# Performance work log

Hardware: AMD Instinct MI355X
Metric: run time of the kernel (lower is better)

The kernel has to match this reference:

```python
import jax, jax.numpy as jnp
import numpy as np

FFT_LEN = 256
WIN_LEN = 768
FRM_LEN = 128
PPF_TAP = WIN_LEN // FFT_LEN  # 6
SCALE = -256.0
GROUP_DELAY = 648  # module uses group_delay = -648
B, C, S, T = 8, 2, FFT_LEN // 2 + 1, 4096


def _make_lpf(win_len):
    # firwin(win_len, 0.5, window='hann', scale=False) equivalent
    n = np.arange(win_len, dtype=np.float64)
    w = 0.5 - 0.5 * np.cos(2.0 * np.pi * n / (win_len - 1))
    h = w * np.sinc(0.5 * (n - (win_len - 1) / 2.0))
    return jnp.asarray(h, dtype=jnp.float32)


def setup_inputs() -> dict:
    key = jax.random.key(0)
    k1, k2 = jax.random.split(key)
    spectrum_real = jax.random.normal(k1, (B, C, S, T), dtype=jnp.float32)
    spectrum_imag = jax.random.normal(k2, (B, C, S, T), dtype=jnp.float32)
    lpf_coef = _make_lpf(WIN_LEN)
    return {"spectrum_real": spectrum_real, "spectrum_imag": spectrum_imag, "lpf_coef": lpf_coef}


def reference(spectrum_real, spectrum_imag, lpf_coef):
    # spectrum: (B, C, S, T) complex; per-frame irfft over subbands
    spec = jnp.swapaxes(spectrum_real + 1j * spectrum_imag, -1, -2)  # (B,C,T,S)
    fftout = jnp.fft.irfft(spec, n=FFT_LEN, axis=-1)                 # (B,C,T,FFT_LEN)
    rev = fftout[..., ::-1]                                          # comp_in[fft_len-j-1]
    v = jnp.tile(rev, (1, 1, 1, PPF_TAP)) * lpf_coef                 # (B,C,T,WIN_LEN)
    b, c, t, _ = v.shape
    num_samples = t * FRM_LEN
    # overlap-add: frame t contributes v[t] at offset t*FRM_LEN (shifting buffer recurrence)
    idx = jnp.arange(t)[:, None] * FRM_LEN + jnp.arange(WIN_LEN)[None, :]  # (T, WIN_LEN)
    y = jnp.zeros((b, c, num_samples + WIN_LEN), dtype=v.dtype)
    y = y.at[..., idx].add(v)[..., :num_samples]
    y = y * (FRM_LEN * SCALE)
    # circular shift by group delay, then trim the wrapped tail
    y = jnp.roll(y, -GROUP_DELAY, axis=-1)[..., :-GROUP_DELAY]
    return y
```

## Files before the change

kernel.cpp:

```cpp
#include <hip/hip_runtime.h>
#include <hip/hip_bf16.h>
#include <math.h>

#define NBINS   129
#define NFFT    256
#define WINL    768
#define TFRAMES 4096
#define OUTL    523640
#define NQUADS  (OUTL / 4)
#define SHIFT   648
#define WSEG    26
#define CHUNK   (WSEG * 128)
#define NCHUNK  ((OUTL + CHUNK - 1) / CHUNK)
#define FF      64
#define FFS     32

#define KDIM    288
#define KROW    296
#define GROW    268
#define WBYTES  (16 * 9 * 64 * 16)
#define GBYTES  ((size_t)16 * TFRAMES * 256 * 2)
#define NSTG    17
#define NF4     9

typedef __attribute__((ext_vector_type(8))) short bf16x8;
typedef __attribute__((ext_vector_type(4))) float f32x4;

static __device__ __forceinline__ ushort f2bf(float x) {
    union { float f; unsigned u; } v; v.f = x;
    unsigned r = v.u + 0x7FFFu + ((v.u >> 16) & 1u);
    return (ushort)(r >> 16);
}
static __device__ __forceinline__ float bf2f(ushort u) {
    union { unsigned u_; float f; } g; g.u_ = ((unsigned)u) << 16; return g.f;
}

__global__ void build_w_kernel(ushort* __restrict__ wp)
{
    const int gid  = blockIdx.x * 256 + threadIdx.x;
    const int lane = gid & 63;
    const int mtks = gid >> 6;
    const int ks   = mtks % 9;
    const int mt   = mtks / 9;
    const int m    = mt * 16 + (lane & 15);
    const int kb   = ks * 32 + ((lane >> 4) << 3);

    ushort o[8];
    #pragma unroll
    for (int e = 0; e < 8; ++e) {
        const int kap = kb + e;
        float val = 0.f;
        if (kap < 258) {
            const int k = kap >> 1;
            float s, c;
            sincospif((float)(k * (m + 1)) * (1.0f / 128.0f), &s, &c);
            if (kap & 1)  val = (k >= 1 && k <= 127) ? s * (2.0f / 256.0f) : 0.f;
            else          val = (k == 0 || k == 128) ? c * (1.0f / 256.0f)
                                                     : c * (2.0f / 256.0f);
        }
        o[e] = f2bf(val);
    }
    int4 pk;
    pk.x = o[0] | (o[1] << 16); pk.y = o[2] | (o[3] << 16);
    pk.z = o[4] | (o[5] << 16); pk.w = o[6] | (o[7] << 16);
    ((int4*)wp)[gid] = pk;
}

__global__ __launch_bounds__(256, 4)
void pfb_dft_kernel(const float* __restrict__ gre, const float* __restrict__ gim,
                    const ushort* __restrict__ wp, ushort* __restrict__ Gg)
{
    __shared__ ushort s_Bu[FF * KROW];

    const int t0  = blockIdx.x * FF;
    const int bc  = blockIdx.y;
    const int tid = threadIdx.x;
    const size_t specBase = (size_t)bc * NBINS * TFRAMES;

    const float4* gre4 = (const float4*)(gre + specBase);
    const float4* gim4 = (const float4*)(gim + specBase);
    float4 vr4[NF4], vi4[NF4];
    #pragma unroll
    for (int r = 0; r < NF4; ++r) {
        const int idx4 = tid + r * 256;
        float4 a = {0.f, 0.f, 0.f, 0.f}, b = {0.f, 0.f, 0.f, 0.f};
        if (idx4 < NBINS * (FF / 4)) {
            const int k = idx4 >> 4, f4 = idx4 & 15;
            const size_t o4 = (size_t)k * (TFRAMES / 4) + (size_t)(t0 >> 2) + f4;
            a = gre4[o4]; b = gim4[o4];
        }
        vr4[r] = a; vi4[r] = b;
    }
    #pragma unroll
    for (int r = 0; r < NF4; ++r) {
        const int idx4 = tid + r * 256;
        if (idx4 < NBINS * (FF / 4)) {
            const int k = idx4 >> 4, f4 = idx4 & 15;
            const float rr[4] = {vr4[r].x, vr4[r].y, vr4[r].z, vr4[r].w};
            const float ii[4] = {vi4[r].x, vi4[r].y, vi4[r].z, vi4[r].w};
            #pragma unroll
            for (int j = 0; j < 4; ++j) {
                __hip_bfloat162 p = __float22bfloat162_rn(make_float2(rr[j], ii[j]));
                *(__hip_bfloat162*)&s_Bu[(4 * f4 + j) * KROW + 2 * k] = p;
            }
        }
    }
    for (int idx = tid; idx < FF * (KROW - 258); idx += 256) {
        const int f = idx / (KROW - 258), r2 = idx - f * (KROW - 258);
        s_Bu[f * KROW + 258 + r2] = 0;
    }
    __syncthreads();

    const int lane = tid & 63;
    const int wid  = tid >> 6;
    const int brow = lane & 15;
    const int kgrp = (lane >> 4) << 3;

    f32x4 acc[4][4];
    #pragma unroll
    for (int mi = 0; mi < 4; ++mi)
        #pragma unroll
        for (int nt = 0; nt < 4; ++nt)
            acc[mi][nt] = (f32x4){0.f, 0.f, 0.f, 0.f};

    const ushort* wbase0 = wp + ((size_t)(wid * 4) * 9 * 64 + (size_t)lane) * 8;
    #pragma unroll
    for (int ks = 0; ks < 9; ++ks) {
        bf16x8 bv[4];
        #pragma unroll
        for (int nt = 0; nt < 4; ++nt)
            bv[nt] = *(const bf16x8*)&s_Bu[(nt * 16 + brow) * KROW + ks * 32 + kgrp];
        #pragma unroll
        for (int mi = 0; mi < 4; ++mi) {
            const bf16x8 aw = *(const bf16x8*)(wbase0 + mi * 4608 + ks * 512);
            #pragma unroll
            for (int nt = 0; nt < 4; ++nt)
                acc[mi][nt] = __builtin_amdgcn_mfma_f32_16x16x32_bf16(aw, bv[nt], acc[mi][nt], 0, 0, 0);
        }
    }

    ushort* gout = Gg + ((size_t)bc * TFRAMES + t0) * NFFT;
    #pragma unroll
    for (int mi = 0; mi < 4; ++mi) {
        const int m0 = (wid * 4 + mi) * 16 + ((lane >> 4) << 2);
        #pragma unroll
        for (int nt = 0; nt < 4; ++nt) {
            const int f = nt * 16 + brow;
            __hip_bfloat162 lo = __float22bfloat162_rn(make_float2(acc[mi][nt].x, acc[mi][nt].y));
            __hip_bfloat162 hi = __float22bfloat162_rn(make_float2(acc[mi][nt].z, acc[mi][nt].w));
            uint2 pk; pk.x = *(unsigned*)&lo; pk.y = *(unsigned*)&hi;
            *(uint2*)&gout[f * NFFT + m0] = pk;
        }
    }
}

__global__ __launch_bounds__(256, 8)
void pfb_oa_kernel(const ushort* __restrict__ Gg, const float* __restrict__ glpf,
                   float* __restrict__ out)
{
    const int tid = threadIdx.x;
    const int bc  = blockIdx.y;
    const int h0  = blockIdx.x * 512 + tid;

    const int b = (4 * h0 + SHIFT) & 127;
    float4 lw[6];
    #pragma unroll
    for (int p = 0; p < 6; ++p) lw[p] = *(const float4*)&glpf[(p << 7) + b];

    const ushort* Gb = Gg + (size_t)bc * TFRAMES * NFFT;
    const size_t outBase = (size_t)bc * OUTL;

    #pragma unroll
    for (int j = 0; j < 2; ++j) {
        const int h = h0 + j * 256;
        int a = (4 * h + SHIFT) >> 7;
        if (a > TFRAMES - 1) a = TFRAMES - 1;
        float s0 = 0.f, s1 = 0.f, s2 = 0.f, s3 = 0.f;
        #pragma unroll
        for (int p = 0; p < 6; ++p) {
            const ushort4 q = *(const ushort4*)&Gb[(size_t)(a - p) * NFFT + b + ((p & 1) << 7)];
            s0 += lw[p].x * bf2f(q.x);
            s1 += lw[p].y * bf2f(q.y);
            s2 += lw[p].z * bf2f(q.z);
            s3 += lw[p].w * bf2f(q.w);
        }
        if (h < NQUADS) {
            float4 o;
            o.x = s0 * (-32768.0f); o.y = s1 * (-32768.0f);
            o.z = s2 * (-32768.0f); o.w = s3 * (-32768.0f);
            *(float4*)&out[outBase + 4 * h] = o;
        }
    }
}

__global__ __launch_bounds__(256, 4)
void pfb_mfma_kernel(const float* __restrict__ gre, const float* __restrict__ gim,
                     const float* __restrict__ glpf, const ushort* __restrict__ wp,
                     float* __restrict__ out)
{
    __shared__ ushort s_bufu[FFS * KROW];
    __shared__ float  s_lpf[WINL];
    ushort* s_Bu = s_bufu;
    ushort (*s_G)[GROW] = (ushort (*)[GROW])s_bufu;

    const int q   = blockIdx.x;
    const int bc  = blockIdx.y;
    const int tid = threadIdx.x;
    const int t0  = WSEG * q;
    const size_t specBase = (size_t)bc * NBINS * TFRAMES;

    for (int idx = tid; idx < WINL; idx += 256) s_lpf[idx] = glpf[idx];

    float vr[NSTG], vi[NSTG];
    #pragma unroll
    for (int r = 0; r < NSTG; ++r) {
        const int idx = tid + r * 256;
        const int k = idx >> 5, f = idx & 31;
        const int t = t0 + f;
        const bool ok = (idx < NBINS * FFS) && (t < TFRAMES);
        float a = 0.f, bb = 0.f;
        if (ok) {
            const size_t g = specBase + (size_t)k * TFRAMES + (size_t)t;
            a = gre[g]; bb = gim[g];
        }
        vr[r] = a; vi[r] = bb;
    }
    #pragma unroll
    for (int r = 0; r < NSTG; ++r) {
        const int idx = tid + r * 256;
        if (idx < NBINS * FFS) {
            const int k = idx >> 5, f = idx & 31;
            __hip_bfloat162 p = __float22bfloat162_rn(make_float2(vr[r], vi[r]));
            *(__hip_bfloat162*)&s_Bu[f * KROW + 2 * k] = p;
        }
    }
    for (int idx = tid; idx < FFS * (KROW - 258); idx += 256) {
        const int f = idx / (KROW - 258), r = idx - f * (KROW - 258);
        s_Bu[f * KROW + 258 + r] = 0;
    }
    __syncthreads();

    const int lane = tid & 63;
    const int wid  = tid >> 6;
    const int brow = lane & 15;
    const int kgrp = (lane >> 4) << 3;

    bf16x8 bfrag[2][9];
    #pragma unroll
    for (int nt = 0; nt < 2; ++nt)
        #pragma unroll
        for (int ks = 0; ks < 9; ++ks)
            bfrag[nt][ks] = *(const bf16x8*)&s_Bu[(nt * 16 + brow) * KROW + ks * 32 + kgrp];

    f32x4 acc[4][2];
    #pragma unroll
    for (int mi = 0; mi < 4; ++mi)
        #pragma unroll
        for (int nt = 0; nt < 2; ++nt)
            acc[mi][nt] = (f32x4){0.f, 0.f, 0.f, 0.f};

    #pragma unroll 1
    for (int mi = 0; mi < 4; ++mi) {
        const ushort* wbase = wp + ((size_t)((wid * 4 + mi) * 9) * 64 + lane) * 8;
        #pragma unroll
        for (int ks = 0; ks < 9; ++ks) {
            const bf16x8 aw = *(const bf16x8*)(wbase + ks * 512);
            acc[mi][0] = __builtin_amdgcn_mfma_f32_16x16x32_bf16(aw, bfrag[0][ks], acc[mi][0], 0, 0, 0);
            acc[mi][1] = __builtin_amdgcn_mfma_f32_16x16x32_bf16(aw, bfrag[1][ks], acc[mi][1], 0, 0, 0);
        }
    }
    __syncthreads();

    #pragma unroll
    for (int mi = 0; mi < 4; ++mi) {
        const int m0 = (wid * 4 + mi) * 16 + ((lane >> 4) << 2);
        #pragma unroll
        for (int nt = 0; nt < 2; ++nt) {
            const int f = nt * 16 + brow;
            __hip_bfloat162 lo = __float22bfloat162_rn(make_float2(acc[mi][nt].x, acc[mi][nt].y));
            __hip_bfloat162 hi = __float22bfloat162_rn(make_float2(acc[mi][nt].z, acc[mi][nt].w));
            uint2 pk; pk.x = *(unsigned*)&lo; pk.y = *(unsigned*)&hi;
            *(uint2*)&s_G[f][m0] = pk;
        }
    }
    __syncthreads();

    const size_t outBase = (size_t)bc * OUTL;
    const int i0 = q * CHUNK;
    #pragma unroll 1
    for (int r = 0; r < 13; ++r) {
        const int i = i0 + r * 256 + tid;
        const int s = i + SHIFT;
        const int tlo = (s - 640) >> 7;
        int thi = s >> 7;
        if (thi > t0 + FFS - 1) thi = t0 + FFS - 1;
        if (thi > TFRAMES - 1) thi = TFRAMES - 1;
        float sum = 0.f;
        #pragma unroll
        for (int u = 0; u < 6; ++u) {
            const int t  = tlo + u;
            int jj = s - (t << 7);
            if (jj < 0) jj = 0;
            const float w = s_lpf[jj];
            sum += (t <= thi) ? w * bf2f(s_G[t - t0][jj & 255]) : 0.f;
        }
        if (i < OUTL) out[outBase + i] = sum * (-32768.0f);
    }
}

extern "C" void kernel_launch(void* const* d_in, const int* in_sizes, int n_in,
                              void* d_out, int out_size, void* d_ws, size_t ws_size,
                              hipStream_t stream)
{
    const float* gre  = (const float*)d_in[0];
    const float* gim  = (const float*)d_in[1];
    const float* glpf = (const float*)d_in[2];
    float* out = (float*)d_out;

    if (ws_size >= (size_t)WBYTES + GBYTES) {
        ushort* wp = (ushort*)d_ws;
        ushort* Gg = (ushort*)((char*)d_ws + WBYTES);
        build_w_kernel<<<36, 256, 0, stream>>>(wp);
        dim3 gridA(TFRAMES / FF, 16);
        pfb_dft_kernel<<<gridA, 256, 0, stream>>>(gre, gim, wp, Gg);
        dim3 gridB((NQUADS + 511) / 512, 16);
        pfb_oa_kernel<<<gridB, 256, 0, stream>>>(Gg, glpf, out);
    } else if (ws_size >= (size_t)WBYTES) {
        ushort* wp = (ushort*)d_ws;
        build_w_kernel<<<36, 256, 0, stream>>>(wp);
        dim3 grid(NCHUNK, 16);
        pfb_mfma_kernel<<<grid, 256, 0, stream>>>(gre, gim, glpf, wp, out);
    }
}
```

Baseline: 52.45 us.

## Load DFT spectrum operands directly from global memory, dropping the LDS staging

The DFT kernel no longer stages the spectrum tile in shared memory. Each lane now gathers its own real/imag values straight from global memory inside the MFMA k-loop and converts them to bf16 pairs in registers. This removes the LDS writes, the zero padding and the block barrier. In exchange it issues many scalar, strided global loads: each of the 4 nt tiles reads 16 consecutive frames in a k row, and every k row is fetched redundantly by all four waves. Occupancy is also lowered to 3 blocks per CU, presumably for register pressure. Indices are clamped at 128, which relies on the matching weights being zero for padded k.

```diff
diff --git a/kernel.cpp b/kernel.cpp
--- a/kernel.cpp
+++ b/kernel.cpp
@@ -21,7 +21,6 @@
 #define WBYTES  (16 * 9 * 64 * 16)
 #define GBYTES  ((size_t)16 * TFRAMES * 256 * 2)
 #define NSTG    17
-#define NF4     9
 
 typedef __attribute__((ext_vector_type(8))) short bf16x8;
 typedef __attribute__((ext_vector_type(4))) float f32x4;
@@ -66,55 +65,20 @@
     ((int4*)wp)[gid] = pk;
 }
 
-__global__ __launch_bounds__(256, 4)
+__global__ __launch_bounds__(256, 3)
 void pfb_dft_kernel(const float* __restrict__ gre, const float* __restrict__ gim,
                     const ushort* __restrict__ wp, ushort* __restrict__ Gg)
 {
-    __shared__ ushort s_Bu[FF * KROW];
-
     const int t0  = blockIdx.x * FF;
     const int bc  = blockIdx.y;
     const int tid = threadIdx.x;
-    const size_t specBase = (size_t)bc * NBINS * TFRAMES;
-
-    const float4* gre4 = (const float4*)(gre + specBase);
-    const float4* gim4 = (const float4*)(gim + specBase);
-    float4 vr4[NF4], vi4[NF4];
-    #pragma unroll
-    for (int r = 0; r < NF4; ++r) {
-        const int idx4 = tid + r * 256;
-        float4 a = {0.f, 0.f, 0.f, 0.f}, b = {0.f, 0.f, 0.f, 0.f};
-        if (idx4 < NBINS * (FF / 4)) {
-            const int k = idx4 >> 4, f4 = idx4 & 15;
-            const size_t o4 = (size_t)k * (TFRAMES / 4) + (size_t)(t0 >> 2) + f4;
-            a = gre4[o4]; b = gim4[o4];
-        }
-        vr4[r] = a; vi4[r] = b;
-    }
-    #pragma unroll
-    for (int r = 0; r < NF4; ++r) {
-        const int idx4 = tid + r * 256;
-        if (idx4 < NBINS * (FF / 4)) {
-            const int k = idx4 >> 4, f4 = idx4 & 15;
-            const float rr[4] = {vr4[r].x, vr4[r].y, vr4[r].z, vr4[r].w};
-            const float ii[4] = {vi4[r].x, vi4[r].y, vi4[r].z, vi4[r].w};
-            #pragma unroll
-            for (int j = 0; j < 4; ++j) {
-                __hip_bfloat162 p = __float22bfloat162_rn(make_float2(rr[j], ii[j]));
-                *(__hip_bfloat162*)&s_Bu[(4 * f4 + j) * KROW + 2 * k] = p;
-            }
-        }
-    }
-    for (int idx = tid; idx < FF * (KROW - 258); idx += 256) {
-        const int f = idx / (KROW - 258), r2 = idx - f * (KROW - 258);
-        s_Bu[f * KROW + 258 + r2] = 0;
-    }
-    __syncthreads();
-
     const int lane = tid & 63;
     const int wid  = tid >> 6;
     const int brow = lane & 15;
-    const int kgrp = (lane >> 4) << 3;
+    const int kq   = lane >> 4;
+    const size_t specBase = (size_t)bc * NBINS * TFRAMES;
+    const float* __restrict__ reB = gre + specBase + t0;
+    const float* __restrict__ imB = gim + specBase + t0;
 
     f32x4 acc[4][4];
     #pragma unroll
@@ -124,25 +88,43 @@
             acc[mi][nt] = (f32x4){0.f, 0.f, 0.f, 0.f};
 
     const ushort* wbase0 = wp + ((size_t)(wid * 4) * 9 * 64 + (size_t)lane) * 8;
+
     #pragma unroll
     for (int ks = 0; ks < 9; ++ks) {
+        const int k0 = ks * 16 + kq * 4;
+        bf16x8 aw[4];
+        #pragma unroll
+        for (int mi = 0; mi < 4; ++mi)
+            aw[mi] = *(const bf16x8*)(wbase0 + mi * 4608 + ks * 512);
+
         bf16x8 bv[4];
         #pragma unroll
-        for (int nt = 0; nt < 4; ++nt)
-            bv[nt] = *(const bf16x8*)&s_Bu[(nt * 16 + brow) * KROW + ks * 32 + kgrp];
-        #pragma unroll
-        for (int mi = 0; mi < 4; ++mi) {
-            const bf16x8 aw = *(const bf16x8*)(wbase0 + mi * 4608 + ks * 512);
+        for (int nt = 0; nt < 4; ++nt) {
+            const int t = nt * 16 + brow;
+            union { bf16x8 v; unsigned u[4]; } pk;
+            #pragma unroll
+            for (int j = 0; j < 4; ++j) {
+                const int k = (k0 + j <= 128) ? (k0 + j) : 128;
+                const size_t off = (size_t)k * TFRAMES + (size_t)t;
+                const float re = reB[off];
+                const float im = imB[off];
+                __hip_bfloat162 p = __float22bfloat162_rn(make_float2(re, im));
+                pk.u[j] = *(unsigned*)&p;
+            }
+            bv[nt] = pk.v;
+        }
+
+        #pragma unroll
+        for (int mi = 0; mi < 4; ++mi)
             #pragma unroll
             for (int nt = 0; nt < 4; ++nt)
-                acc[mi][nt] = __builtin_amdgcn_mfma_f32_16x16x32_bf16(aw, bv[nt], acc[mi][nt], 0, 0, 0);
-        }
+                acc[mi][nt] = __builtin_amdgcn_mfma_f32_16x16x32_bf16(aw[mi], bv[nt], acc[mi][nt], 0, 0, 0);
     }
 
     ushort* gout = Gg + ((size_t)bc * TFRAMES + t0) * NFFT;
     #pragma unroll
     for (int mi = 0; mi < 4; ++mi) {
-        const int m0 = (wid * 4 + mi) * 16 + ((lane >> 4) << 2);
+        const int m0 = (wid * 4 + mi) * 16 + (kq << 2);
         #pragma unroll
         for (int nt = 0; nt < 4; ++nt) {
             const int f = nt * 16 + brow;
```

After: 54.59 us. +4.1%, slower.
